# Kernel optimization log

Hardware: AMD Instinct MI355X
Metric: run time of the kernel (lower is better)

## Reference

```python
import jax, jax.numpy as jnp
import numpy as np

B, N, C, DP, H, P = 1, 1024, 384, 128, 12, 4
EPS = 1e-5


def setup_inputs() -> dict:
    key = jax.random.key(0)
    ks = jax.random.split(key, 16)
    def w(k, shape, fan_in):
        return (jax.random.normal(k, shape, dtype=jnp.float32) / np.sqrt(fan_in)).astype(jnp.float32)
    return {
        "single": jax.random.normal(ks[0], (B, N, C), dtype=jnp.float32),
        "pair": jax.random.normal(ks[1], (B, N, N, DP), dtype=jnp.float32),
        "rotations": jax.random.normal(ks[2], (B, N, 3, 3), dtype=jnp.float32),
        "translations": jax.random.normal(ks[3], (B, N, 3), dtype=jnp.float32),
        "Wq": w(ks[4], (C, C), C), "bq": jnp.zeros((C,), jnp.float32),
        "Wk": w(ks[5], (C, C), C), "bk": jnp.zeros((C,), jnp.float32),
        "Wv": w(ks[6], (C, C), C), "bv": jnp.zeros((C,), jnp.float32),
        "Wp": w(ks[7], (DP, H), DP), "bp": jnp.zeros((H,), jnp.float32),
        "Wpq": w(ks[8], (C, H * 3 * P), C), "bpq": jnp.zeros((H * 3 * P,), jnp.float32),
        "Wpk": w(ks[9], (C, H * 3 * P), C), "bpk": jnp.zeros((H * 3 * P,), jnp.float32),
        "Wo": w(ks[10], (C, C), C), "bo": jnp.zeros((C,), jnp.float32),
        "gamma": jnp.ones((C,), jnp.float32), "beta": jnp.zeros((C,), jnp.float32),
    }


def reference(single, pair, rotations, translations, Wq, bq, Wk, bk, Wv, bv,
              Wp, bp, Wpq, bpq, Wpk, bpk, Wo, bo, gamma, beta):
    b, n, c = single.shape
    h, p = H, P
    scaling = (c // h) ** (-0.5)

    # scalar q/k/v: [B,N,H,C/H]
    q = (single @ Wq + bq).reshape(b, n, h, c // h)
    k = (single @ Wk + bk).reshape(b, n, h, c // h)
    v = (single @ Wv + bv).reshape(b, n, h, c // h)

    # pair bias: [B,H,N,N]
    pair_bias = jnp.einsum('bnmd,dh->bhnm', pair, Wp) + bp[None, :, None, None]

    # local point q/k: [B,N,H,3,P]; rotate xyz axis into global frame
    q_pts = (single @ Wpq + bpq).reshape(b, n, h, 3, p)
    k_pts = (single @ Wpk + bpk).reshape(b, n, h, 3, p)
    qg = jnp.einsum('bnyx,bnhxp->bnhyp', rotations, q_pts)  # [B,N,H,3,P]
    kg = jnp.einsum('bnyx,bnhxp->bnhyp', rotations, k_pts)

    # squared-distance logits: -0.5 * ||qg_i - kg_j||^2 summed over (xyz, P)
    sq = jnp.sum(qg * qg, axis=(-1, -2))  # [B,N,H]
    sk = jnp.sum(kg * kg, axis=(-1, -2))  # [B,N,H]
    qk_pts = jnp.einsum('bnhxp,bmhxp->bhnm', qg, kg)
    point_logits = -0.5 * (jnp.transpose(sq, (0, 2, 1))[:, :, :, None]
                           + jnp.transpose(sk, (0, 2, 1))[:, :, None, :]
                           - 2.0 * qk_pts) * scaling  # [B,H,N,N]

    logits = jnp.einsum('bnhc,bmhc->bhnm', q, k) * scaling + pair_bias + point_logits
    attn = jax.nn.softmax(logits, axis=-1)
    weighted = jnp.einsum('bhnm,bmhc->bnhc', attn, v).reshape(b, n, c)
    out = weighted @ Wo + bo

    # LayerNorm(single + out)
    x = single + out
    mu = jnp.mean(x, axis=-1, keepdims=True)
    var = jnp.mean((x - mu) ** 2, axis=-1, keepdims=True)
    return (x - mu) * jax.lax.rsqrt(var + EPS) * gamma + beta
```

## Files before the change

### kernel.cpp

```cpp
#include <hip/hip_runtime.h>
#include <math.h>

#define N 1024
#define C 384
#define H 12
#define DP 128
#define HP 144
#define MT 64
#define NT 16
#define RW 4
#define QBL 16
#define SCALING 0.17677669529663687f
#define LN_EPS 1e-5f

__global__ __launch_bounds__(256) void k_qkv(
    const float* __restrict__ single,
    const float* __restrict__ Wq, const float* __restrict__ bq,
    const float* __restrict__ Wk, const float* __restrict__ bk,
    const float* __restrict__ Wv, const float* __restrict__ bv,
    const float* __restrict__ Wpq, const float* __restrict__ bpq,
    const float* __restrict__ Wpk, const float* __restrict__ bpk,
    float* __restrict__ q, float* __restrict__ kcg, float* __restrict__ v,
    float* __restrict__ qp, float* __restrict__ kp)
{
  __shared__ __align__(16) float A_s[64 * 33];
  __shared__ __align__(16) float B_s[32 * 48];
  int t = threadIdx.x;
  int nt = blockIdx.x, mt = blockIdx.y;
  int m0 = mt * 64;
  const float* W; const float* bias; int ld, kind, cb;
  if (nt < 8)       { W = Wq;  bias = bq;  ld = C;  cb = nt * 48;        kind = 0; }
  else if (nt < 16) { W = Wk;  bias = bk;  ld = C;  cb = (nt - 8) * 48;  kind = 1; }
  else if (nt < 24) { W = Wv;  bias = bv;  ld = C;  cb = (nt - 16) * 48; kind = 2; }
  else if (nt < 27) { W = Wpq; bias = bpq; ld = HP; cb = (nt - 24) * 48; kind = 3; }
  else              { W = Wpk; bias = bpk; ld = HP; cb = (nt - 27) * 48; kind = 4; }
  int tr = t >> 4, tc = t & 15;
  float acc[4][3] = {};
  for (int k0 = 0; k0 < C; k0 += 32) {
    if (k0) __syncthreads();
    #pragma unroll
    for (int i = 0; i < 8; i++) {
      int fi = i * 256 + t; int row = fi >> 5, col = fi & 31;
      A_s[row * 33 + col] = single[(m0 + row) * C + k0 + col];
    }
    #pragma unroll
    for (int i = 0; i < 6; i++) {
      int fi = i * 256 + t; int row = fi / 48, col = fi % 48;
      B_s[row * 48 + col] = W[(k0 + row) * ld + cb + col];
    }
    __syncthreads();
    #pragma unroll
    for (int k = 0; k < 32; k++) {
      float a[4], b[3];
      #pragma unroll
      for (int r = 0; r < 4; r++) a[r] = A_s[(tr * 4 + r) * 33 + k];
      #pragma unroll
      for (int c = 0; c < 3; c++) b[c] = B_s[k * 48 + tc * 3 + c];
      #pragma unroll
      for (int r = 0; r < 4; r++)
        #pragma unroll
        for (int c = 0; c < 3; c++) acc[r][c] = fmaf(a[r], b[c], acc[r][c]);
    }
  }
  #pragma unroll
  for (int c = 0; c < 3; c++) {
    int col = cb + tc * 3 + c;
    float bb = bias[col];
    #pragma unroll
    for (int r = 0; r < 4; r++) {
      int row = m0 + tr * 4 + r;
      float val = acc[r][c] + bb;
      if (kind == 0)      q[row * C + col] = val;
      else if (kind == 1) kcg[((col >> 5) * N + row) * 48 + (col & 31)] = val;
      else if (kind == 2) v[row * C + col] = val;
      else if (kind == 3) qp[row * HP + col] = val;
      else                kp[row * HP + col] = val;
    }
  }
}

__global__ __launch_bounds__(256) void k_rot(
    const float* __restrict__ qp, const float* __restrict__ kp,
    const float* __restrict__ rot,
    float* __restrict__ qg, float* __restrict__ kcg,
    float* __restrict__ sq, float* __restrict__ sknh)
{
  __shared__ __align__(16) float qp_s[HP], kp_s[HP], rot_s[9], q2_s[HP], k2_s[HP];
  int n = blockIdx.x, t = threadIdx.x;
  if (t < HP) { qp_s[t] = qp[n * HP + t]; kp_s[t] = kp[n * HP + t]; }
  if (t < 9)  rot_s[t] = rot[n * 9 + t];
  __syncthreads();
  if (t < HP) {
    int h = t / 12, r12 = t % 12, y = r12 >> 2, p = r12 & 3;
    float qgv = rot_s[y*3] * qp_s[h*12 + p] + rot_s[y*3+1] * qp_s[h*12 + 4 + p]
              + rot_s[y*3+2] * qp_s[h*12 + 8 + p];
    float kgv = rot_s[y*3] * kp_s[h*12 + p] + rot_s[y*3+1] * kp_s[h*12 + 4 + p]
              + rot_s[y*3+2] * kp_s[h*12 + 8 + p];
    qg[n * HP + t] = qgv;
    kcg[(h * N + n) * 48 + 32 + r12] = kgv;
    q2_s[t] = qgv * qgv; k2_s[t] = kgv * kgv;
  }
  if (t < 48) kcg[((t >> 2) * N + n) * 48 + 44 + (t & 3)] = 0.f;
  __syncthreads();
  if (t < H) {
    float s1 = 0.f, s2 = 0.f;
    #pragma unroll
    for (int e = 0; e < 12; e++) { s1 += q2_s[t * 12 + e]; s2 += k2_s[t * 12 + e]; }
    sq[n * H + t] = s1; sknh[n * H + t] = s2;
  }
}

__global__ __launch_bounds__(256) void k_pb(
    const float4* __restrict__ pair4, const float* __restrict__ Wp,
    const float* __restrict__ bp, const float* __restrict__ sq,
    const float* __restrict__ sknh, float* __restrict__ pb)
{
  __shared__ __align__(16) float wp_s[12 * 128];
  __shared__ __align__(16) float ob_s[12][128];
  __shared__ float sq_s[12], bp_s[12];
  int t = threadIdx.x;
  int bid = blockIdx.x;
  int n = bid >> 3;
  int m0 = (bid & 7) * 128;
  #pragma unroll
  for (int i = 0; i < 6; i++) {
    int fi = i * 256 + t; int h = fi >> 7, d = fi & 127;
    wp_s[h * 128 + d] = Wp[d * 12 + h];
  }
  if (t < 12) { sq_s[t] = sq[n * 12 + t]; bp_s[t] = bp[t]; }
  __syncthreads();
  int tc = t & 3, rid = t >> 2;
  long rowA = (long)n * N + m0 + rid;
  const float4* rpA = pair4 + rowA * 32;
  const float4* rpB = rpA + 64 * 32;
  const float4* w4 = (const float4*)wp_s;
  float accA[12] = {}, accB[12] = {};
  #pragma unroll
  for (int i = 0; i < 8; i++) {
    float4 a = rpA[i * 4 + tc];
    float4 b = rpB[i * 4 + tc];
    #pragma unroll
    for (int h = 0; h < 12; h++) {
      float4 w = w4[h * 32 + i * 4 + tc];
      accA[h] = fmaf(a.x, w.x, accA[h]);
      accA[h] = fmaf(a.y, w.y, accA[h]);
      accA[h] = fmaf(a.z, w.z, accA[h]);
      accA[h] = fmaf(a.w, w.w, accA[h]);
      accB[h] = fmaf(b.x, w.x, accB[h]);
      accB[h] = fmaf(b.y, w.y, accB[h]);
      accB[h] = fmaf(b.z, w.z, accB[h]);
      accB[h] = fmaf(b.w, w.w, accB[h]);
    }
  }
  #pragma unroll
  for (int h = 0; h < 12; h++) {
    accA[h] += __shfl_xor(accA[h], 1);
    accA[h] += __shfl_xor(accA[h], 2);
    accB[h] += __shfl_xor(accB[h], 1);
    accB[h] += __shfl_xor(accB[h], 2);
  }
  if (tc == 0) {
    float skrA[12], skrB[12];
    #pragma unroll
    for (int i = 0; i < 3; i++) {
      *(float4*)&skrA[i * 4] = *(const float4*)&sknh[(m0 + rid) * 12 + i * 4];
      *(float4*)&skrB[i * 4] = *(const float4*)&sknh[(m0 + 64 + rid) * 12 + i * 4];
    }
    #pragma unroll
    for (int h = 0; h < 12; h++) {
      ob_s[h][rid]      = accA[h] + bp_s[h] - 0.5f * SCALING * (sq_s[h] + skrA[h]);
      ob_s[h][64 + rid] = accB[h] + bp_s[h] - 0.5f * SCALING * (sq_s[h] + skrB[h]);
    }
  }
  __syncthreads();
  #pragma unroll
  for (int i = 0; i < 6; i++) {
    int idx = i * 256 + t; int h = idx >> 7, r = idx & 127;
    pb[(long)h * (N * (long)N) + (long)n * N + m0 + r] = ob_s[h][r];
  }
}

__global__ __launch_bounds__(256) void k_attn(
    const float* __restrict__ q, const float* __restrict__ qg,
    const float* __restrict__ kcg, const float* __restrict__ v,
    const float* __restrict__ pb, float* __restrict__ wt)
{
  __shared__ __align__(16) float kc_s[64 * 64];
  __shared__ __align__(16) float v_s[32 * 64];
  __shared__ __align__(16) float qc_s[QBL][48];
  __shared__ __align__(16) float p_s[4][RW][MT];

  int t = threadIdx.x;
  int bid = blockIdx.x;
  int s = (bid & 7) * 96 + (bid >> 3);
  int h = s >> 6, qb = s & 63;
  int q0 = qb * QBL;
  int w = t >> 6, lane = t & 63;
  long pbbase = (long)h * (N * (long)N);
  const float* kch = kcg + (long)h * N * 48;
  int hc32 = h * 32;
  int mr = t >> 3, cq = t & 7;

  float4 pk0, pk1, pk2, pv0, pv1;
  float pb_cur[RW], pb_nxt[RW];

#define STAGE_LOAD(M0) \
  { int f0 = t, f1 = 256 + t, f2 = 512 + t; \
    pk0 = *(const float4*)&kch[((M0) + f0 / 12) * 48 + (f0 % 12) * 4]; \
    pk1 = *(const float4*)&kch[((M0) + f1 / 12) * 48 + (f1 % 12) * 4]; \
    pk2 = *(const float4*)&kch[((M0) + f2 / 12) * 48 + (f2 % 12) * 4]; \
    pv0 = *(const float4*)&v[((M0) + mr) * C + hc32 + cq * 4]; \
    pv1 = *(const float4*)&v[((M0) + 32 + mr) * C + hc32 + cq * 4]; }

#define ST_KC(F, VAL) \
  { int row_ = (F) / 12, c4_ = (F) % 12; \
    *(float4*)&kc_s[row_ * 64 + ((c4_ ^ (row_ & 7)) << 2)] = VAL; }
#define ST_V1(MM, CC, VV) \
  v_s[(CC) * 64 + ((((MM) >> 2) ^ ((CC) & 7)) << 2) + ((MM) & 3)] = VV;
#define ST_V(MM, VAL) \
  { ST_V1(MM, cq * 4 + 0, VAL.x) ST_V1(MM, cq * 4 + 1, VAL.y) \
    ST_V1(MM, cq * 4 + 2, VAL.z) ST_V1(MM, cq * 4 + 3, VAL.w) }

#define STAGE_WRITE() \
  { ST_KC(t, pk0) ST_KC(256 + t, pk1) ST_KC(512 + t, pk2) \
    ST_V(mr, pv0) ST_V(32 + mr, pv1) }

  STAGE_LOAD(0);
  #pragma unroll
  for (int r = 0; r < RW; r++)
    pb_cur[r] = pb[pbbase + (long)(q0 + w * RW + r) * N + lane];
  if (t < QBL * 12) {
    int r = t / 12, c4 = t % 12;
    float4 val;
    if (c4 < 8)       val = *(const float4*)&q[(q0 + r) * C + hc32 + c4 * 4];
    else if (c4 < 11) val = *(const float4*)&qg[(q0 + r) * HP + h * 12 + (c4 - 8) * 4];
    else              val = make_float4(0.f, 0.f, 0.f, 0.f);
    val.x *= SCALING; val.y *= SCALING; val.z *= SCALING; val.w *= SCALING;
    *(float4*)&qc_s[r][c4 * 4] = val;
  }
  STAGE_WRITE();
  __syncthreads();

  float lsum[RW] = {}, o[RW] = {};
  int cc = lane & 31, seg = lane >> 5;

  for (int tile = 0; tile < NT; tile++) {
    int m0 = tile * MT;
    if (tile < NT - 1) {
      STAGE_LOAD(m0 + MT);
      #pragma unroll
      for (int r = 0; r < RW; r++)
        pb_nxt[r] = pb[pbbase + (long)(q0 + w * RW + r) * N + m0 + MT + lane];
    }
    float L[RW];
    #pragma unroll
    for (int r = 0; r < RW; r++) L[r] = pb_cur[r];
    #pragma unroll
    for (int c4 = 0; c4 < 11; c4++) {
      float4 kv = *(const float4*)&kc_s[lane * 64 + ((c4 ^ (lane & 7)) << 2)];
      #pragma unroll
      for (int r = 0; r < RW; r++) {
        float4 qv = *(const float4*)&qc_s[w * RW + r][c4 * 4];
        L[r] = fmaf(qv.x, kv.x, L[r]);
        L[r] = fmaf(qv.y, kv.y, L[r]);
        L[r] = fmaf(qv.z, kv.z, L[r]);
        L[r] = fmaf(qv.w, kv.w, L[r]);
      }
    }
    #pragma unroll
    for (int r = 0; r < RW; r++) {
      float p = __expf(L[r]);
      lsum[r] += p;
      p_s[w][r][lane] = p;
    }
    #pragma unroll
    for (int j4 = 0; j4 < 8; j4++) {
      float4 vv = *(const float4*)&v_s[cc * 64 + (((seg * 8 + j4) ^ (cc & 7)) << 2)];
      #pragma unroll
      for (int r = 0; r < RW; r++) {
        float4 pv = *(const float4*)&p_s[w][r][seg * 32 + j4 * 4];
        o[r] = fmaf(pv.x, vv.x, o[r]);
        o[r] = fmaf(pv.y, vv.y, o[r]);
        o[r] = fmaf(pv.z, vv.z, o[r]);
        o[r] = fmaf(pv.w, vv.w, o[r]);
      }
    }
    __syncthreads();
    if (tile < NT - 1) {
      STAGE_WRITE();
      #pragma unroll
      for (int r = 0; r < RW; r++) pb_cur[r] = pb_nxt[r];
    }
    __syncthreads();
  }
  #pragma unroll
  for (int r = 0; r < RW; r++) {
    float ls = lsum[r];
    #pragma unroll
    for (int off = 32; off; off >>= 1) ls += __shfl_xor(ls, off);
    float ov = o[r] + __shfl_xor(o[r], 32);
    if (lane < 32) wt[(q0 + w * RW + r) * C + hc32 + lane] = ov / ls;
  }
#undef STAGE_LOAD
#undef STAGE_WRITE
#undef ST_KC
#undef ST_V
#undef ST_V1
}

__global__ __launch_bounds__(384) void k_out(
    const float* __restrict__ wt, const float* __restrict__ Wo,
    const float* __restrict__ bo, const float* __restrict__ single,
    const float* __restrict__ gamma, const float* __restrict__ beta,
    float* __restrict__ out)
{
  __shared__ __align__(16) float wt_s[4 * C];
  __shared__ __align__(16) float red[4][2][6];
  int t = threadIdx.x, n0 = blockIdx.x * 4;
  for (int idx = t; idx < 4 * C; idx += 384) wt_s[idx] = wt[n0 * C + idx];
  __syncthreads();
  float acc[4] = {};
  for (int ck = 0; ck < C; ck++) {
    float w = Wo[ck * C + t];
    #pragma unroll
    for (int i = 0; i < 4; i++) acc[i] = fmaf(wt_s[i * C + ck], w, acc[i]);
  }
  float x[4], bov = bo[t];
  #pragma unroll
  for (int i = 0; i < 4; i++) x[i] = single[(n0 + i) * C + t] + acc[i] + bov;
  int wid = t >> 6, lane = t & 63;
  #pragma unroll
  for (int i = 0; i < 4; i++) {
    float s = x[i], s2 = x[i] * x[i];
    #pragma unroll
    for (int off = 32; off; off >>= 1) { s += __shfl_xor(s, off); s2 += __shfl_xor(s2, off); }
    if (lane == 0) { red[i][0][wid] = s; red[i][1][wid] = s2; }
  }
  __syncthreads();
  float gv = gamma[t], bv = beta[t];
  #pragma unroll
  for (int i = 0; i < 4; i++) {
    float S = 0.f, S2 = 0.f;
    #pragma unroll
    for (int w = 0; w < 6; w++) { S += red[i][0][w]; S2 += red[i][1][w]; }
    float mu = S * (1.0f / C);
    float var = S2 * (1.0f / C) - mu * mu;
    out[(n0 + i) * C + t] = (x[i] - mu) * rsqrtf(var + LN_EPS) * gv + bv;
  }
}

extern "C" void kernel_launch(void* const* d_in, const int* in_sizes, int n_in,
                              void* d_out, int out_size, void* d_ws, size_t ws_size,
                              hipStream_t stream) {
  const float* single = (const float*)d_in[0];
  const float* pair   = (const float*)d_in[1];
  const float* rot    = (const float*)d_in[2];
  const float* Wq  = (const float*)d_in[4];  const float* bq  = (const float*)d_in[5];
  const float* Wk  = (const float*)d_in[6];  const float* bk  = (const float*)d_in[7];
  const float* Wv  = (const float*)d_in[8];  const float* bv  = (const float*)d_in[9];
  const float* Wp  = (const float*)d_in[10]; const float* bp  = (const float*)d_in[11];
  const float* Wpq = (const float*)d_in[12]; const float* bpq = (const float*)d_in[13];
  const float* Wpk = (const float*)d_in[14]; const float* bpk = (const float*)d_in[15];
  const float* Wo  = (const float*)d_in[16]; const float* bo  = (const float*)d_in[17];
  const float* gamma = (const float*)d_in[18]; const float* beta = (const float*)d_in[19];

  float* ws   = (float*)d_ws;
  float* pb   = ws;
  float* q    = pb + 12L * N * N;
  float* v    = q + N * C;
  float* qp   = v + N * C;
  float* kp   = qp + N * HP;
  float* qg   = kp + N * HP;
  float* kcg  = qg + N * HP;
  float* sq   = kcg + 12L * N * 48;
  float* sknh = sq + N * H;
  float* wt   = sknh + N * H;

  k_qkv<<<dim3(30, 16), 256, 0, stream>>>(single, Wq, bq, Wk, bk, Wv, bv,
                                          Wpq, bpq, Wpk, bpk, q, kcg, v, qp, kp);
  k_rot<<<N, 256, 0, stream>>>(qp, kp, rot, qg, kcg, sq, sknh);
  k_pb<<<8192, 256, 0, stream>>>((const float4*)pair, Wp, bp, sq, sknh, pb);
  k_attn<<<768, 256, 0, stream>>>(q, qg, kcg, v, pb, wt);
  k_out<<<256, 384, 0, stream>>>(wt, Wo, bo, single, gamma, beta, (float*)d_out);
}
```

Baseline: 277.7 us.

## Restructure attention to read K/V per lane from global, drop LDS staging

The attention kernel no longer stages key and value tiles through shared memory with double buffering and barriers. Each lane instead loads its own key row and value row directly from global memory into registers, computes logits for two queries, and accumulates a full 32-wide output per lane, with a shared-memory transpose reduction at the end. The query block size is halved and the grid doubled to raise parallelism. This removes the per-tile syncs and LDS traffic, but cuts K/V reuse across queries from four rows per wave to two, so global and L2 traffic rises, and register pressure from the 64 accumulators may limit occupancy.

```diff
diff --git a/kernel.cpp b/kernel.cpp
--- a/kernel.cpp
+++ b/kernel.cpp
@@ -8,8 +8,7 @@
 #define HP 144
 #define MT 64
 #define NT 16
-#define RW 4
-#define QBL 16
+#define QBL 8
 #define SCALING 0.17677669529663687f
 #define LN_EPS 1e-5f
 
@@ -180,55 +179,22 @@
   }
 }
 
-__global__ __launch_bounds__(256) void k_attn(
+__global__ __launch_bounds__(256, 3) void k_attn(
     const float* __restrict__ q, const float* __restrict__ qg,
     const float* __restrict__ kcg, const float* __restrict__ v,
     const float* __restrict__ pb, float* __restrict__ wt)
 {
-  __shared__ __align__(16) float kc_s[64 * 64];
-  __shared__ __align__(16) float v_s[32 * 64];
   __shared__ __align__(16) float qc_s[QBL][48];
-  __shared__ __align__(16) float p_s[4][RW][MT];
+  __shared__ __align__(16) float red_s[4][32][65];
 
   int t = threadIdx.x;
   int bid = blockIdx.x;
-  int s = (bid & 7) * 96 + (bid >> 3);
-  int h = s >> 6, qb = s & 63;
+  int s = (bid & 7) * 192 + (bid >> 3);
+  int h = s >> 7, qb = s & 127;
   int q0 = qb * QBL;
   int w = t >> 6, lane = t & 63;
-  long pbbase = (long)h * (N * (long)N);
-  const float* kch = kcg + (long)h * N * 48;
   int hc32 = h * 32;
-  int mr = t >> 3, cq = t & 7;
-
-  float4 pk0, pk1, pk2, pv0, pv1;
-  float pb_cur[RW], pb_nxt[RW];
-
-#define STAGE_LOAD(M0) \
-  { int f0 = t, f1 = 256 + t, f2 = 512 + t; \
-    pk0 = *(const float4*)&kch[((M0) + f0 / 12) * 48 + (f0 % 12) * 4]; \
-    pk1 = *(const float4*)&kch[((M0) + f1 / 12) * 48 + (f1 % 12) * 4]; \
-    pk2 = *(const float4*)&kch[((M0) + f2 / 12) * 48 + (f2 % 12) * 4]; \
-    pv0 = *(const float4*)&v[((M0) + mr) * C + hc32 + cq * 4]; \
-    pv1 = *(const float4*)&v[((M0) + 32 + mr) * C + hc32 + cq * 4]; }
-
-#define ST_KC(F, VAL) \
-  { int row_ = (F) / 12, c4_ = (F) % 12; \
-    *(float4*)&kc_s[row_ * 64 + ((c4_ ^ (row_ & 7)) << 2)] = VAL; }
-#define ST_V1(MM, CC, VV) \
-  v_s[(CC) * 64 + ((((MM) >> 2) ^ ((CC) & 7)) << 2) + ((MM) & 3)] = VV;
-#define ST_V(MM, VAL) \
-  { ST_V1(MM, cq * 4 + 0, VAL.x) ST_V1(MM, cq * 4 + 1, VAL.y) \
-    ST_V1(MM, cq * 4 + 2, VAL.z) ST_V1(MM, cq * 4 + 3, VAL.w) }
-
-#define STAGE_WRITE() \
-  { ST_KC(t, pk0) ST_KC(256 + t, pk1) ST_KC(512 + t, pk2) \
-    ST_V(mr, pv0) ST_V(32 + mr, pv1) }
-
-  STAGE_LOAD(0);
-  #pragma unroll
-  for (int r = 0; r < RW; r++)
-    pb_cur[r] = pb[pbbase + (long)(q0 + w * RW + r) * N + lane];
+
   if (t < QBL * 12) {
     int r = t / 12, c4 = t % 12;
     float4 val;
@@ -238,74 +204,70 @@
     val.x *= SCALING; val.y *= SCALING; val.z *= SCALING; val.w *= SCALING;
     *(float4*)&qc_s[r][c4 * 4] = val;
   }
-  STAGE_WRITE();
-  __syncthreads();
-
-  float lsum[RW] = {}, o[RW] = {};
-  int cc = lane & 31, seg = lane >> 5;
+  __syncthreads();
+
+  const float4* kcb = (const float4*)kcg + (long)h * N * 12;
+  const float4* vb  = (const float4*)v + h * 8;
+  const float*  pbp = pb + (long)h * (N * (long)N) + (long)(q0 + w * 2) * N + lane;
+
+  float lsum[2] = {};
+  float o_[2][32] = {};
 
   for (int tile = 0; tile < NT; tile++) {
-    int m0 = tile * MT;
-    if (tile < NT - 1) {
-      STAGE_LOAD(m0 + MT);
-      #pragma unroll
-      for (int r = 0; r < RW; r++)
-        pb_nxt[r] = pb[pbbase + (long)(q0 + w * RW + r) * N + m0 + MT + lane];
-    }
-    float L[RW];
-    #pragma unroll
-    for (int r = 0; r < RW; r++) L[r] = pb_cur[r];
+    int m = tile * MT + lane;
+    const float4* kcr = kcb + m * 12;
+    float4 kr[11];
+    #pragma unroll
+    for (int j = 0; j < 11; j++) kr[j] = kcr[j];
+    float L0 = pbp[tile * MT];
+    float L1 = pbp[N + tile * MT];
     #pragma unroll
     for (int c4 = 0; c4 < 11; c4++) {
-      float4 kv = *(const float4*)&kc_s[lane * 64 + ((c4 ^ (lane & 7)) << 2)];
-      #pragma unroll
-      for (int r = 0; r < RW; r++) {
-        float4 qv = *(const float4*)&qc_s[w * RW + r][c4 * 4];
-        L[r] = fmaf(qv.x, kv.x, L[r]);
-        L[r] = fmaf(qv.y, kv.y, L[r]);
-        L[r] = fmaf(qv.z, kv.z, L[r]);
-        L[r] = fmaf(qv.w, kv.w, L[r]);
-      }
-    }
-    #pragma unroll
-    for (int r = 0; r < RW; r++) {
-      float p = __expf(L[r]);
-      lsum[r] += p;
-      p_s[w][r][lane] = p;
-    }
-    #pragma unroll
-    for (int j4 = 0; j4 < 8; j4++) {
-      float4 vv = *(const float4*)&v_s[cc * 64 + (((seg * 8 + j4) ^ (cc & 7)) << 2)];
-      #pragma unroll
-      for (int r = 0; r < RW; r++) {
-        float4 pv = *(const float4*)&p_s[w][r][seg * 32 + j4 * 4];
-        o[r] = fmaf(pv.x, vv.x, o[r]);
-        o[r] = fmaf(pv.y, vv.y, o[r]);
-        o[r] = fmaf(pv.z, vv.z, o[r]);
-        o[r] = fmaf(pv.w, vv.w, o[r]);
-      }
-    }
-    __syncthreads();
-    if (tile < NT - 1) {
-      STAGE_WRITE();
-      #pragma unroll
-      for (int r = 0; r < RW; r++) pb_cur[r] = pb_nxt[r];
-    }
-    __syncthreads();
-  }
-  #pragma unroll
-  for (int r = 0; r < RW; r++) {
-    float ls = lsum[r];
-    #pragma unroll
-    for (int off = 32; off; off >>= 1) ls += __shfl_xor(ls, off);
-    float ov = o[r] + __shfl_xor(o[r], 32);
-    if (lane < 32) wt[(q0 + w * RW + r) * C + hc32 + lane] = ov / ls;
-  }
-#undef STAGE_LOAD
-#undef STAGE_WRITE
-#undef ST_KC
-#undef ST_V
-#undef ST_V1
+      float4 qv0 = *(const float4*)&qc_s[w * 2][c4 * 4];
+      float4 qv1 = *(const float4*)&qc_s[w * 2 + 1][c4 * 4];
+      L0 = fmaf(qv0.x, kr[c4].x, L0);
+      L0 = fmaf(qv0.y, kr[c4].y, L0);
+      L0 = fmaf(qv0.z, kr[c4].z, L0);
+      L0 = fmaf(qv0.w, kr[c4].w, L0);
+      L1 = fmaf(qv1.x, kr[c4].x, L1);
+      L1 = fmaf(qv1.y, kr[c4].y, L1);
+      L1 = fmaf(qv1.z, kr[c4].z, L1);
+      L1 = fmaf(qv1.w, kr[c4].w, L1);
+    }
+    float p0 = __expf(L0), p1 = __expf(L1);
+    lsum[0] += p0; lsum[1] += p1;
+    const float4* vr = vb + (long)m * 96;
+    #pragma unroll
+    for (int j = 0; j < 8; j++) {
+      float4 vv = vr[j];
+      o_[0][j * 4 + 0] = fmaf(p0, vv.x, o_[0][j * 4 + 0]);
+      o_[0][j * 4 + 1] = fmaf(p0, vv.y, o_[0][j * 4 + 1]);
+      o_[0][j * 4 + 2] = fmaf(p0, vv.z, o_[0][j * 4 + 2]);
+      o_[0][j * 4 + 3] = fmaf(p0, vv.w, o_[0][j * 4 + 3]);
+      o_[1][j * 4 + 0] = fmaf(p1, vv.x, o_[1][j * 4 + 0]);
+      o_[1][j * 4 + 1] = fmaf(p1, vv.y, o_[1][j * 4 + 1]);
+      o_[1][j * 4 + 2] = fmaf(p1, vv.z, o_[1][j * 4 + 2]);
+      o_[1][j * 4 + 3] = fmaf(p1, vv.w, o_[1][j * 4 + 3]);
+    }
+  }
+
+  #pragma unroll
+  for (int off = 32; off; off >>= 1) {
+    lsum[0] += __shfl_xor(lsum[0], off);
+    lsum[1] += __shfl_xor(lsum[1], off);
+  }
+  int li = lane & 31, half = lane >> 5;
+  #pragma unroll
+  for (int r = 0; r < 2; r++) {
+    #pragma unroll
+    for (int cc = 0; cc < 32; cc++) red_s[w][cc][lane] = o_[r][cc];
+    float sred = 0.f;
+    #pragma unroll
+    for (int i = 0; i < 32; i++) sred += red_s[w][li][half * 32 + i];
+    sred += __shfl_xor(sred, 32);
+    if (lane < 32)
+      wt[(q0 + w * 2 + r) * C + hc32 + lane] = sred / lsum[r];
+  }
 }
 
 __global__ __launch_bounds__(384) void k_out(
@@ -380,6 +342,6 @@
                                           Wpq, bpq, Wpk, bpk, q, kcg, v, qp, kp);
   k_rot<<<N, 256, 0, stream>>>(qp, kp, rot, qg, kcg, sq, sknh);
   k_pb<<<8192, 256, 0, stream>>>((const float4*)pair, Wp, bp, sq, sknh, pb);
-  k_attn<<<768, 256, 0, stream>>>(q, qg, kcg, v, pb, wt);
+  k_attn<<<1536, 256, 0, stream>>>(q, qg, kcg, v, pb, wt);
   k_out<<<256, 384, 0, stream>>>(wt, Wo, bo, single, gamma, beta, (float*)d_out);
 }
```

After: 395.5 us. 42.4% more time.
